# Performance work log

Measured on AMD Instinct MI355X. Metric: run time of the kernel, lower is better.

## Reference

```python
import jax, jax.numpy as jnp
import numpy as np

H = 4096   # hidden_dim
I = 4096   # input_dim
V = 32000  # output_size


def setup_inputs() -> dict:
    key = jax.random.key(0)
    ks = jax.random.split(key, 16)
    s_x = 1.0 / np.sqrt(I)
    s_h = 1.0 / np.sqrt(H)
    inp = {
        'prev_h': jax.random.normal(ks[0], (H,), jnp.float32),
        'prev_c': jax.random.normal(ks[1], (H,), jnp.float32),
        'x_t': jax.random.normal(ks[2], (I,), jnp.float32),
        'w_xf': jax.random.normal(ks[3], (H, I), jnp.float32) * s_x,
        'w_hf': jax.random.normal(ks[4], (H, H), jnp.float32) * s_h,
        'b_f': jnp.zeros((H,), jnp.float32),
        'w_xi': jax.random.normal(ks[5], (H, I), jnp.float32) * s_x,
        'w_hi': jax.random.normal(ks[6], (H, H), jnp.float32) * s_h,
        'b_i': jnp.zeros((H,), jnp.float32),
        'w_xg': jax.random.normal(ks[7], (H, I), jnp.float32) * s_x,
        'w_hg': jax.random.normal(ks[8], (H, H), jnp.float32) * s_h,
        'b_g': jnp.zeros((H,), jnp.float32),
        'w_xo': jax.random.normal(ks[9], (H, I), jnp.float32) * s_x,
        'w_ho': jax.random.normal(ks[10], (H, H), jnp.float32) * s_h,
        'b_o': jnp.zeros((H,), jnp.float32),
        'w_hy': jax.random.normal(ks[11], (V, H), jnp.float32) * s_h,
        'b_y': jnp.zeros((V,), jnp.float32),
    }
    return inp


def reference(prev_h, prev_c, x_t,
              w_xf, w_hf, b_f,
              w_xi, w_hi, b_i,
              w_xg, w_hg, b_g,
              w_xo, w_ho, b_o,
              w_hy, b_y):
    # Fuse the 8 small matvecs into 2 stacked matvecs: [4H, I] @ x and [4H, H] @ h.
    W_x = jnp.concatenate([w_xf, w_xi, w_xg, w_xo], axis=0)  # [4H, I]
    W_h = jnp.concatenate([w_hf, w_hi, w_hg, w_ho], axis=0)  # [4H, H]
    b = jnp.concatenate([b_f, b_i, b_g, b_o], axis=0)        # [4H]
    gates = W_x @ x_t + W_h @ prev_h + b                      # [4H]
    f_t = jax.nn.sigmoid(gates[0:H])
    i_t = jax.nn.sigmoid(gates[H:2 * H])
    g_t = jnp.tanh(gates[2 * H:3 * H])
    o_t = jax.nn.sigmoid(gates[3 * H:4 * H])
    c_t = f_t * prev_c + i_t * g_t
    h_t = o_t * jnp.tanh(c_t)
    y_t = jax.nn.softmax(w_hy @ h_t + b_y, axis=-1)           # [V]
    return (h_t, c_t, y_t)
```

## Files before the change

kernel.cpp:

```cpp
#include <hip/hip_runtime.h>
#include <math.h>

#define HDIM 4096
#define VDIM 32000

__device__ inline float wave_reduce_sum(float v) {
    #pragma unroll
    for (int off = 32; off > 0; off >>= 1)
        v += __shfl_down(v, off, 64);
    return v;
}

__device__ inline float wave_reduce_max(float v) {
    #pragma unroll
    for (int off = 32; off > 0; off >>= 1)
        v = fmaxf(v, __shfl_down(v, off, 64));
    return v;
}

__global__ __launch_bounds__(256) void lstm_gates_kernel(
    const float* __restrict__ prev_h, const float* __restrict__ prev_c,
    const float* __restrict__ x_t,
    const float* __restrict__ w_xf, const float* __restrict__ w_hf, const float* __restrict__ b_f,
    const float* __restrict__ w_xi, const float* __restrict__ w_hi, const float* __restrict__ b_i,
    const float* __restrict__ w_xg, const float* __restrict__ w_hg, const float* __restrict__ b_g,
    const float* __restrict__ w_xo, const float* __restrict__ w_ho, const float* __restrict__ b_o,
    float* __restrict__ out)
{
    const int row  = blockIdx.x;
    const int wave = threadIdx.x >> 6;
    const int lane = threadIdx.x & 63;

    const float* wx; const float* wh; const float* bb;
    if      (wave == 0) { wx = w_xf; wh = w_hf; bb = b_f; }
    else if (wave == 1) { wx = w_xi; wh = w_hi; bb = b_i; }
    else if (wave == 2) { wx = w_xg; wh = w_hg; bb = b_g; }
    else                { wx = w_xo; wh = w_ho; bb = b_o; }
    wx += (size_t)row * HDIM;
    wh += (size_t)row * HDIM;

    float acc = 0.f;
    #pragma unroll 4
    for (int j = lane * 4; j < HDIM; j += 64 * 4) {
        float4 a = *reinterpret_cast<const float4*>(wx + j);
        float4 v = *reinterpret_cast<const float4*>(x_t + j);
        acc += a.x * v.x + a.y * v.y + a.z * v.z + a.w * v.w;
        float4 b = *reinterpret_cast<const float4*>(wh + j);
        float4 u = *reinterpret_cast<const float4*>(prev_h + j);
        acc += b.x * u.x + b.y * u.y + b.z * u.z + b.w * u.w;
    }
    acc = wave_reduce_sum(acc);

    __shared__ float g4[4];
    if (lane == 0) g4[wave] = acc + bb[row];
    __syncthreads();
    if (threadIdx.x == 0) {
        float ft = 1.f / (1.f + expf(-g4[0]));
        float it = 1.f / (1.f + expf(-g4[1]));
        float gt = tanhf(g4[2]);
        float ot = 1.f / (1.f + expf(-g4[3]));
        float c  = ft * prev_c[row] + it * gt;
        float h  = ot * tanhf(c);
        out[row]        = h;
        out[HDIM + row] = c;
    }
}

__global__ __launch_bounds__(256) void logits_kernel(
    const float* __restrict__ w_hy, const float* __restrict__ b_y,
    const float* __restrict__ h, float* __restrict__ logits)
{
    const int row  = blockIdx.x * 4 + (threadIdx.x >> 6);
    const int lane = threadIdx.x & 63;
    const float* w = w_hy + (size_t)row * HDIM;

    float acc = 0.f;
    #pragma unroll 4
    for (int j = lane * 4; j < HDIM; j += 64 * 4) {
        float4 a = *reinterpret_cast<const float4*>(w + j);
        float4 v = *reinterpret_cast<const float4*>(h + j);
        acc += a.x * v.x + a.y * v.y + a.z * v.z + a.w * v.w;
    }
    acc = wave_reduce_sum(acc);
    if (lane == 0) logits[row] = acc + b_y[row];
}

__global__ __launch_bounds__(1024) void softmax_stats_kernel(
    const float* __restrict__ logits, float* __restrict__ stats)
{
    __shared__ float sm[16];
    const int tid = threadIdx.x;

    float m = -INFINITY;
    for (int i = tid; i < VDIM; i += 1024) m = fmaxf(m, logits[i]);
    m = wave_reduce_max(m);
    if ((tid & 63) == 0) sm[tid >> 6] = m;
    __syncthreads();
    if (tid < 16) {
        m = sm[tid];
        #pragma unroll
        for (int off = 8; off > 0; off >>= 1) m = fmaxf(m, __shfl_down(m, off, 64));
        if (tid == 0) sm[0] = m;
    }
    __syncthreads();
    m = sm[0];
    __syncthreads();

    float s = 0.f;
    for (int i = tid; i < VDIM; i += 1024) s += expf(logits[i] - m);
    s = wave_reduce_sum(s);
    __shared__ float sm2[16];
    if ((tid & 63) == 0) sm2[tid >> 6] = s;
    __syncthreads();
    if (tid < 16) {
        s = sm2[tid];
        #pragma unroll
        for (int off = 8; off > 0; off >>= 1) s += __shfl_down(s, off, 64);
        if (tid == 0) { stats[0] = m; stats[1] = 1.f / s; }
    }
}

__global__ __launch_bounds__(256) void softmax_norm_kernel(
    const float* __restrict__ logits, const float* __restrict__ stats,
    float* __restrict__ y)
{
    const int i = blockIdx.x * 256 + threadIdx.x;
    if (i < VDIM) y[i] = expf(logits[i] - stats[0]) * stats[1];
}

extern "C" void kernel_launch(void* const* d_in, const int* in_sizes, int n_in,
                              void* d_out, int out_size, void* d_ws, size_t ws_size,
                              hipStream_t stream)
{
    const float* prev_h = (const float*)d_in[0];
    const float* prev_c = (const float*)d_in[1];
    const float* x_t    = (const float*)d_in[2];
    const float* w_xf   = (const float*)d_in[3];
    const float* w_hf   = (const float*)d_in[4];
    const float* b_f    = (const float*)d_in[5];
    const float* w_xi   = (const float*)d_in[6];
    const float* w_hi   = (const float*)d_in[7];
    const float* b_i    = (const float*)d_in[8];
    const float* w_xg   = (const float*)d_in[9];
    const float* w_hg   = (const float*)d_in[10];
    const float* b_g    = (const float*)d_in[11];
    const float* w_xo   = (const float*)d_in[12];
    const float* w_ho   = (const float*)d_in[13];
    const float* b_o    = (const float*)d_in[14];
    const float* w_hy   = (const float*)d_in[15];
    const float* b_y    = (const float*)d_in[16];

    float* out = (float*)d_out;
    float* h_t = out;
    float* y_t = out + 2 * HDIM;

    float* logits = (float*)d_ws;
    float* stats  = logits + VDIM;

    lstm_gates_kernel<<<HDIM, 256, 0, stream>>>(
        prev_h, prev_c, x_t,
        w_xf, w_hf, b_f, w_xi, w_hi, b_i,
        w_xg, w_hg, b_g, w_xo, w_ho, b_o, out);

    logits_kernel<<<VDIM / 4, 256, 0, stream>>>(w_hy, b_y, h_t, logits);

    softmax_stats_kernel<<<1, 1024, 0, stream>>>(logits, stats);

    softmax_norm_kernel<<<(VDIM + 255) / 256, 256, 0, stream>>>(logits, stats, y_t);
}
```

Before: 196.2 us.

## Stage vectors in LDS and parallelize softmax reduction across blocks

Both matvec kernels now copy the shared input vectors (x_t, prev_h, h) into LDS once per block, use two independent accumulators, and the logits loop is widened to two float4 loads per iteration. The single-block softmax stats kernel is replaced by a 125-block partial max/sum kernel followed by a small combine kernel, so the reduction is no longer serialized on one CU. This adds an extra kernel launch and per-block LDS fill cost, and the main cost (streaming the weights from HBM) is unchanged.

```diff
diff --git a/kernel.cpp b/kernel.cpp
--- a/kernel.cpp
+++ b/kernel.cpp
@@ -3,6 +3,7 @@
 
 #define HDIM 4096
 #define VDIM 32000
+#define NPART 125
 
 __device__ inline float wave_reduce_sum(float v) {
     #pragma unroll
@@ -27,6 +28,14 @@
     const float* __restrict__ w_xo, const float* __restrict__ w_ho, const float* __restrict__ b_o,
     float* __restrict__ out)
 {
+    __shared__ float s_x[HDIM];
+    __shared__ float s_h[HDIM];
+    for (int i = threadIdx.x * 4; i < HDIM; i += 256 * 4) {
+        *reinterpret_cast<float4*>(&s_x[i]) = *reinterpret_cast<const float4*>(&x_t[i]);
+        *reinterpret_cast<float4*>(&s_h[i]) = *reinterpret_cast<const float4*>(&prev_h[i]);
+    }
+    __syncthreads();
+
     const int row  = blockIdx.x;
     const int wave = threadIdx.x >> 6;
     const int lane = threadIdx.x & 63;
@@ -39,17 +48,17 @@
     wx += (size_t)row * HDIM;
     wh += (size_t)row * HDIM;
 
-    float acc = 0.f;
+    float accx = 0.f, acch = 0.f;
     #pragma unroll 4
     for (int j = lane * 4; j < HDIM; j += 64 * 4) {
         float4 a = *reinterpret_cast<const float4*>(wx + j);
-        float4 v = *reinterpret_cast<const float4*>(x_t + j);
-        acc += a.x * v.x + a.y * v.y + a.z * v.z + a.w * v.w;
+        float4 v = *reinterpret_cast<const float4*>(&s_x[j]);
+        accx += a.x * v.x + a.y * v.y + a.z * v.z + a.w * v.w;
         float4 b = *reinterpret_cast<const float4*>(wh + j);
-        float4 u = *reinterpret_cast<const float4*>(prev_h + j);
-        acc += b.x * u.x + b.y * u.y + b.z * u.z + b.w * u.w;
+        float4 u = *reinterpret_cast<const float4*>(&s_h[j]);
+        acch += b.x * u.x + b.y * u.y + b.z * u.z + b.w * u.w;
     }
-    acc = wave_reduce_sum(acc);
+    float acc = wave_reduce_sum(accx + acch);
 
     __shared__ float g4[4];
     if (lane == 0) g4[wave] = acc + bb[row];
@@ -70,54 +79,67 @@
     const float* __restrict__ w_hy, const float* __restrict__ b_y,
     const float* __restrict__ h, float* __restrict__ logits)
 {
+    __shared__ float s_h[HDIM];
+    for (int i = threadIdx.x * 4; i < HDIM; i += 256 * 4)
+        *reinterpret_cast<float4*>(&s_h[i]) = *reinterpret_cast<const float4*>(&h[i]);
+    __syncthreads();
+
     const int row  = blockIdx.x * 4 + (threadIdx.x >> 6);
     const int lane = threadIdx.x & 63;
     const float* w = w_hy + (size_t)row * HDIM;
 
-    float acc = 0.f;
+    float acc0 = 0.f, acc1 = 0.f;
     #pragma unroll 4
-    for (int j = lane * 4; j < HDIM; j += 64 * 4) {
+    for (int j = lane * 8; j < HDIM; j += 64 * 8) {
         float4 a = *reinterpret_cast<const float4*>(w + j);
-        float4 v = *reinterpret_cast<const float4*>(h + j);
-        acc += a.x * v.x + a.y * v.y + a.z * v.z + a.w * v.w;
+        float4 v = *reinterpret_cast<const float4*>(&s_h[j]);
+        acc0 += a.x * v.x + a.y * v.y + a.z * v.z + a.w * v.w;
+        float4 b = *reinterpret_cast<const float4*>(w + j + 4);
+        float4 u = *reinterpret_cast<const float4*>(&s_h[j + 4]);
+        acc1 += b.x * u.x + b.y * u.y + b.z * u.z + b.w * u.w;
     }
-    acc = wave_reduce_sum(acc);
+    float acc = wave_reduce_sum(acc0 + acc1);
     if (lane == 0) logits[row] = acc + b_y[row];
 }
 
-__global__ __launch_bounds__(1024) void softmax_stats_kernel(
-    const float* __restrict__ logits, float* __restrict__ stats)
+__global__ __launch_bounds__(256) void softmax_partial_kernel(
+    const float* __restrict__ logits, float2* __restrict__ part)
 {
-    __shared__ float sm[16];
+    const int wave = threadIdx.x >> 6;
+    const int lane = threadIdx.x & 63;
+    float v = logits[blockIdx.x * 256 + threadIdx.x];
+
+    float m = wave_reduce_max(v);
+    __shared__ float sm[4];
+    if (lane == 0) sm[wave] = m;
+    __syncthreads();
+    m = fmaxf(fmaxf(sm[0], sm[1]), fmaxf(sm[2], sm[3]));
+
+    float s = wave_reduce_sum(expf(v - m));
+    __shared__ float ss[4];
+    if (lane == 0) ss[wave] = s;
+    __syncthreads();
+    if (threadIdx.x == 0)
+        part[blockIdx.x] = make_float2(m, ss[0] + ss[1] + ss[2] + ss[3]);
+}
+
+__global__ __launch_bounds__(128) void softmax_combine_kernel(
+    const float2* __restrict__ part, float* __restrict__ stats)
+{
     const int tid = threadIdx.x;
+    float2 p = (tid < NPART) ? part[tid] : make_float2(-1e30f, 0.f);
 
-    float m = -INFINITY;
-    for (int i = tid; i < VDIM; i += 1024) m = fmaxf(m, logits[i]);
-    m = wave_reduce_max(m);
+    float m = wave_reduce_max(p.x);
+    __shared__ float sm[2];
     if ((tid & 63) == 0) sm[tid >> 6] = m;
     __syncthreads();
-    if (tid < 16) {
-        m = sm[tid];
-        #pragma unroll
-        for (int off = 8; off > 0; off >>= 1) m = fmaxf(m, __shfl_down(m, off, 64));
-        if (tid == 0) sm[0] = m;
-    }
+    float M = fmaxf(sm[0], sm[1]);
+
+    float s = wave_reduce_sum(p.y * expf(p.x - M));
+    __shared__ float s2[2];
+    if ((tid & 63) == 0) s2[tid >> 6] = s;
     __syncthreads();
-    m = sm[0];
-    __syncthreads();
-
-    float s = 0.f;
-    for (int i = tid; i < VDIM; i += 1024) s += expf(logits[i] - m);
-    s = wave_reduce_sum(s);
-    __shared__ float sm2[16];
-    if ((tid & 63) == 0) sm2[tid >> 6] = s;
-    __syncthreads();
-    if (tid < 16) {
-        s = sm2[tid];
-        #pragma unroll
-        for (int off = 8; off > 0; off >>= 1) s += __shfl_down(s, off, 64);
-        if (tid == 0) { stats[0] = m; stats[1] = 1.f / s; }
-    }
+    if (tid == 0) { stats[0] = M; stats[1] = 1.f / (s2[0] + s2[1]); }
 }
 
 __global__ __launch_bounds__(256) void softmax_norm_kernel(
@@ -154,8 +176,9 @@
     float* h_t = out;
     float* y_t = out + 2 * HDIM;
 
-    float* logits = (float*)d_ws;
-    float* stats  = logits + VDIM;
+    float*  logits = (float*)d_ws;
+    float*  stats  = logits + VDIM;
+    float2* part   = (float2*)(stats + 2);
 
     lstm_gates_kernel<<<HDIM, 256, 0, stream>>>(
         prev_h, prev_c, x_t,
@@ -164,7 +187,9 @@
 
     logits_kernel<<<VDIM / 4, 256, 0, stream>>>(w_hy, b_y, h_t, logits);
 
-    softmax_stats_kernel<<<1, 1024, 0, stream>>>(logits, stats);
+    softmax_partial_kernel<<<NPART, 256, 0, stream>>>(logits, part);
+
+    softmax_combine_kernel<<<1, 128, 0, stream>>>(part, stats);
 
     softmax_norm_kernel<<<(VDIM + 255) / 256, 256, 0, stream>>>(logits, stats, y_t);
 }
```

New measurement: 190.4 us. 3.0% less time.
